# Kernel optimization log

Measured on AMD Instinct MI355X. Metric: run time of the kernel, lower is better.

## Reference

```python
import jax, jax.numpy as jnp
import numpy as np

S, V, L = 64, 16, 5            # hn_dim=(64,16), num_layers=5
ED, RD, TD = 16, 16, 64        # edge_dim, rbf_dim, t_dim
N, EL, EG, B = 16384, 131072, 262144, 64
FIN = 2 * S + RD + ED          # per-edge message input width
H = S + 2 * V                  # message output: scalar msg + 2 vector gates
CUT_L, CUT_G = 3.0, 10.0


def _ln(x, g, b, eps=1e-5):
    m = x.mean(-1, keepdims=True)
    var = ((x - m) ** 2).mean(-1, keepdims=True)
    return (x - m) / jnp.sqrt(var + eps) * g + b


def _seg_mean(x, idx, n):
    s = jax.ops.segment_sum(x, idx, num_segments=n)
    c = jax.ops.segment_sum(jnp.ones((x.shape[0], 1), x.dtype), idx, num_segments=n)
    return s / jnp.maximum(c, 1.0)


def _edge_geom(ei, pos, cutoff):
    src, tgt = ei[0], ei[1]
    r = pos[tgt] - pos[src]                       # [E,3]
    d = jnp.sqrt(jnp.clip((r * r).sum(-1), 1e-6))
    rn = r / d[:, None]
    centers = jnp.linspace(0.0, cutoff, RD)
    width = cutoff / RD
    env = jnp.where(d < cutoff, 0.5 * (jnp.cos(jnp.pi * d / cutoff) + 1.0), 0.0)
    rbf = jnp.exp(-0.5 * ((d[:, None] - centers) / width) ** 2) * env[:, None]
    return src, tgt, rn, rbf


def setup_inputs() -> dict:
    key = jax.random.key(0)
    ks = iter(jax.random.split(key, 32))
    nrm = lambda shp, sc=1.0: jax.random.normal(next(ks), shp, jnp.float32) * sc
    x = jax.random.randint(next(ks), (N, 3), 0, 16)
    t = nrm((B, TD))
    pos = nrm((N, 3))
    eil = jax.random.randint(next(ks), (2, EL), 0, N)
    eig = jax.random.randint(next(ks), (2, EG), 0, N)
    eal = jax.random.randint(next(ks), (EL,), 0, 5)
    eag = jax.random.randint(next(ks), (EG,), 0, 5)
    batch = jnp.sort(jax.random.randint(next(ks), (N,), 0, B))
    return dict(
        x=x, t=t, pos=pos,
        edge_index_local=eil, edge_index_global=eig,
        edge_attr_local=eal, edge_attr_global=eag, batch=batch,
        atom_emb=nrm((3, 16, S), 0.1),
        bond_emb=nrm((5, ED), 0.1),
        t_w1=nrm((TD, TD), TD ** -0.5), t_b1=jnp.zeros(TD),
        t_w2=nrm((TD, S), TD ** -0.5), t_b2=jnp.zeros(S),
        gnn_wm=nrm((L, 2, FIN, H), FIN ** -0.5), gnn_bm=jnp.zeros((L, 2, H)),
        gnn_wu=nrm((L, 2, S, S), S ** -0.5), gnn_bu=jnp.zeros((L, 2, S)),
        ln_g=jnp.ones((L, S)), ln_b=jnp.zeros((L, S)),
        head_dscore_w=nrm((S, 1), S ** -0.5),
        head_out_w=nrm((V, 1), V ** -0.5),
    )


def reference(x, t, pos, edge_index_local, edge_index_global, edge_attr_local,
              edge_attr_global, batch, atom_emb, bond_emb, t_w1, t_b1, t_w2,
              t_b2, gnn_wm, gnn_bm, gnn_wu, gnn_bu, ln_g, ln_b,
              head_dscore_w, head_out_w):
    n = x.shape[0]
    # AtomEncoder: sum of per-feature-column embeddings; + broadcast t-embedding
    s = atom_emb[0][x[:, 0]] + atom_emb[1][x[:, 1]] + atom_emb[2][x[:, 2]]
    temb = jax.nn.silu(jax.nn.silu(t @ t_w1 + t_b1) @ t_w2 + t_b2)
    s = s + temb[batch]
    v = jnp.zeros((n, 3, V), s.dtype)

    edge_sets = []
    for ei, ea, cut in ((edge_index_local, edge_attr_local, CUT_L),
                        (edge_index_global, edge_attr_global, CUT_G)):
        src, tgt, rn, rbf = _edge_geom(ei, pos, cut)
        edge_sets.append((src, tgt, rn, rbf, bond_emb[ea]))

    for i in range(L):
        for k, (src, tgt, rn, rbf, e) in enumerate(edge_sets):
            feat = jnp.concatenate([s[src], s[tgt], rbf, e], -1)       # [E,FIN]
            h = jax.nn.silu(feat @ gnn_wm[i, k] + gnn_bm[i, k])        # [E,H]
            ms, wv1, wv2 = h[:, :S], h[:, S:S + V], h[:, S + V:]
            vm = v[src] * wv1[:, None, :] + rn[:, :, None] * wv2[:, None, :]
            agg_s = _seg_mean(ms, tgt, n)                              # [N,S]
            agg_v = _seg_mean(vm.reshape(-1, 3 * V), tgt, n).reshape(n, 3, V)
            s = s + jax.nn.silu(agg_s @ gnn_wu[i, k] + gnn_bu[i, k])
            v = v + agg_v
        s = _ln(s, ln_g[i], ln_b[i])

    # ScoreHead (conservative=False)
    dsc = jax.nn.silu(s) @ head_dscore_w                               # [N,1]
    src, tgt = edge_index_global[0], edge_index_global[1]
    sr = (dsc[src] + dsc[tgt]) * (pos[src] - pos[tgt])                 # [E,3]
    sr = jax.ops.segment_sum(sr, tgt, num_segments=n)                  # [N,3]
    score = (v @ head_out_w)[..., 0] + sr                              # [N,3]
    return score
```

## Files before the change

kernel.cpp:

```cpp
#include <hip/hip_runtime.h>
#include <math.h>

#define Sdim 64
#define Vdim 16
#define NLAYER 5
#define EDdim 16
#define RDdim 16
#define TDdim 64
#define FINdim 160
#define Hdim 96
#define NVdim 48
#define ACCW 113
#define HPAD 98
#define VSW 52
#define GW 16

typedef __attribute__((ext_vector_type(8))) short bf16x8;
typedef __attribute__((ext_vector_type(4))) float f32x4;

__device__ __forceinline__ float silu_f(float x) {
    return x / (1.0f + __expf(-x));
}

__device__ __forceinline__ unsigned short f2bf(float x) {
    union { float f; unsigned u; } v; v.f = x;
    unsigned r = v.u + 0x7fffu + ((v.u >> 16) & 1u);
    return (unsigned short)(r >> 16);
}

__global__ __launch_bounds__(256) void pack_kernel(
    const float* __restrict__ wm, const float* __restrict__ bemb,
    unsigned short* __restrict__ wp, unsigned short* __restrict__ bondbf)
{
    int idx = blockIdx.x * 256 + threadIdx.x;
    if (idx < 10 * FINdim * Hdim) {
        int ls = idx / (FINdim * Hdim), rem = idx % (FINdim * Hdim);
        int k = rem / Hdim, c = rem % Hdim;
        wp[(size_t)ls * FINdim * Hdim + ((size_t)(k >> 3) * Hdim + c) * 8 + (k & 7)] =
            f2bf(wm[idx]);
    } else if (idx < 10 * FINdim * Hdim + 80) {
        int i = idx - 10 * FINdim * Hdim;
        bondbf[i] = f2bf(bemb[i]);
    }
}

__global__ __launch_bounds__(64) void temb_kernel(
    const float* __restrict__ t, const float* __restrict__ w1, const float* __restrict__ b1,
    const float* __restrict__ w2, const float* __restrict__ b2, float* __restrict__ temb)
{
    int b = blockIdx.x, j = threadIdx.x;
    __shared__ float row[TDdim];
    __shared__ float hid[TDdim];
    row[j] = t[b * TDdim + j];
    __syncthreads();
    float h = b1[j];
    #pragma unroll 8
    for (int i = 0; i < TDdim; ++i) h = fmaf(row[i], w1[i * TDdim + j], h);
    h = silu_f(h);
    hid[j] = h;
    __syncthreads();
    float o = b2[j];
    #pragma unroll 8
    for (int i = 0; i < TDdim; ++i) o = fmaf(hid[i], w2[i * Sdim + j], o);
    temb[b * Sdim + j] = silu_f(o);
}

__global__ __launch_bounds__(256) void node_init_kernel(
    const int* __restrict__ x, const int* __restrict__ batch,
    const float* __restrict__ aemb, const float* __restrict__ temb,
    float* __restrict__ sfeat, unsigned short* __restrict__ sbf, int n)
{
    int idx = blockIdx.x * 256 + threadIdx.x;
    if (idx >= n * Sdim) return;
    int node = idx >> 6, j = idx & 63;
    int x0 = x[node * 3 + 0], x1 = x[node * 3 + 1], x2 = x[node * 3 + 2];
    float v = aemb[(0 * 16 + x0) * Sdim + j] + aemb[(16 + x1) * Sdim + j]
            + aemb[(32 + x2) * Sdim + j] + temb[batch[node] * Sdim + j];
    sfeat[idx] = v;
    sbf[idx]   = f2bf(v);
}

__global__ __launch_bounds__(256) void count_kernel(
    const int* __restrict__ ei, int E, int* __restrict__ counts)
{
    int e = blockIdx.x * 256 + threadIdx.x;
    if (e >= E) return;
    atomicAdd(&counts[ei[E + e]], 1);
}

__global__ __launch_bounds__(256) void scan_kernel(
    const int* __restrict__ counts, int n,
    int* __restrict__ rowStart, int* __restrict__ cursor)
{
    __shared__ int partial[256];
    __shared__ int spart[257];
    int t = threadIdx.x;
    int chunk = n / 256;
    int base = t * chunk;
    int s = 0;
    for (int i = 0; i < chunk; ++i) s += counts[base + i];
    partial[t] = s;
    __syncthreads();
    if (t == 0) {
        int a = 0;
        for (int i = 0; i < 256; ++i) { spart[i] = a; a += partial[i]; }
        spart[256] = a;
    }
    __syncthreads();
    int off = spart[t];
    for (int i = 0; i < chunk; ++i) {
        rowStart[base + i] = off;
        cursor[base + i]   = off;
        off += counts[base + i];
    }
    if (t == 255) rowStart[n] = spart[256];
}

__global__ __launch_bounds__(256) void scatter_kernel(
    const int* __restrict__ ei, const int* __restrict__ ea, int E,
    int* __restrict__ cursor, int2* __restrict__ st2, int* __restrict__ eaS)
{
    int e = blockIdx.x * 256 + threadIdx.x;
    if (e >= E) return;
    int tgt = ei[E + e];
    int p = atomicAdd(&cursor[tgt], 1);
    st2[p] = make_int2(ei[e], tgt);
    eaS[p] = ea[e];
}

__global__ __launch_bounds__(256) void geom_kernel(
    const float* __restrict__ pos,
    const int2* __restrict__ st2, const int* __restrict__ eaS,
    const unsigned short* __restrict__ bondbf,
    float4* __restrict__ rn4, unsigned short* __restrict__ rbfb,
    int E, float cutoff)
{
    int e = blockIdx.x * 256 + threadIdx.x;
    if (e >= E) return;
    int2 st = st2[e];
    int s = st.x, t = st.y;
    float rx = pos[3*t]-pos[3*s], ry = pos[3*t+1]-pos[3*s+1], rz = pos[3*t+2]-pos[3*s+2];
    float d = sqrtf(fmaxf(rx*rx + ry*ry + rz*rz, 1e-6f));
    float invd = 1.0f / d;
    rn4[e] = make_float4(rx*invd, ry*invd, rz*invd, d);
    float env = (d < cutoff) ? 0.5f * (__cosf(3.14159265358979f * d / cutoff) + 1.0f) : 0.0f;
    float invw = (float)RDdim / cutoff;
    unsigned int pk[8];
    #pragma unroll
    for (int i2 = 0; i2 < 8; ++i2) {
        float c0 = cutoff * ((float)(2*i2)     / 15.0f);
        float c1 = cutoff * ((float)(2*i2 + 1) / 15.0f);
        float t0 = (d - c0) * invw, t1 = (d - c1) * invw;
        unsigned short b0 = f2bf(__expf(-0.5f * t0 * t0) * env);
        unsigned short b1 = f2bf(__expf(-0.5f * t1 * t1) * env);
        pk[i2] = (unsigned)b0 | ((unsigned)b1 << 16);
    }
    uint4* o = reinterpret_cast<uint4*>(rbfb + (size_t)e * 32);
    o[0] = make_uint4(pk[0], pk[1], pk[2], pk[3]);
    o[1] = make_uint4(pk[4], pk[5], pk[6], pk[7]);
    int ea = eaS[e];
    const uint4* bp = reinterpret_cast<const uint4*>(bondbf + ea * EDdim);
    o[2] = bp[0];
    o[3] = bp[1];
}

__global__ __launch_bounds__(192, 4) void fused_layer_tri(
    const float* __restrict__ s_in, float* __restrict__ s_out,
    const unsigned short* __restrict__ sbf_in, unsigned short* __restrict__ sbf_out,
    const float* __restrict__ v_in, float* __restrict__ v_out,
    const int* __restrict__ rowStart,
    const int2* __restrict__ st2,
    const float4* __restrict__ rn4, const unsigned short* __restrict__ rbfb,
    const unsigned short* __restrict__ wp, const float* __restrict__ bg,
    const float* __restrict__ wu, const float* __restrict__ bu,
    const float* __restrict__ lng, const float* __restrict__ lnb,
    int do_ln)
{
    __shared__ float accL[GW * ACCW];
    __shared__ __align__(16) float hS[16 * HPAD];
    __shared__ __align__(16) float vS[16 * VSW];
    __shared__ __align__(16) float rnS[16 * 4];
    __shared__ int rsW[3][GW + 1];

    const int tid  = threadIdx.x;
    const int lane = tid & 63;
    const int wid  = __builtin_amdgcn_readfirstlane(tid >> 6);
    const int l15  = lane & 15, l4 = lane >> 4;
    const int n0   = blockIdx.x * GW;

    bf16x8 B0[5], B1[5];
    #pragma unroll
    for (int kk = 0; kk < 5; ++kk) {
        B0[kk] = *reinterpret_cast<const bf16x8*>(
            wp + ((size_t)(kk * 4 + l4) * Hdim + (wid * 2 + 0) * 16 + l15) * 8);
        B1[kk] = *reinterpret_cast<const bf16x8*>(
            wp + ((size_t)(kk * 4 + l4) * Hdim + (wid * 2 + 1) * 16 + l15) * 8);
    }
    const float bias0 = bg[(wid * 2 + 0) * 16 + l15];
    const float bias1 = bg[(wid * 2 + 1) * 16 + l15];

    if (wid < 2) {
        if (lane < 32)
            #pragma unroll
            for (int i = 0; i < GW; ++i) accL[i * ACCW + wid * 32 + lane] = 0.0f;
    } else if (lane < 49) {
        #pragma unroll
        for (int i = 0; i < GW; ++i) accL[i * ACCW + 64 + lane] = 0.0f;
    }
    if (lane <= GW) rsW[wid][lane] = rowStart[n0 + lane];

    const int eW0 = __builtin_amdgcn_readfirstlane(rsW[wid][0]);
    const int eW1 = __builtin_amdgcn_readfirstlane(rsW[wid][GW]);
    const int eLast = max(eW1 - 1, 0);

    auto reduceChunk = [&](int pb) {
        const int pv = min(16, eW1 - pb);
        if (wid < 2) {
            if (lane < 32) {
                const int col = wid * 32 + lane;
                for (int i = 0; i < GW; ++i) {
                    int lo = rsW[wid][i] - pb;     if (lo < 0) lo = 0;
                    int hi = rsW[wid][i + 1] - pb; if (hi > pv) hi = pv;
                    if (lo >= hi) continue;
                    float msum = 0.0f;
                    for (int e2 = lo; e2 < hi; ++e2) msum += hS[e2 * HPAD + col];
                    accL[i * ACCW + col] += msum;
                }
            }
        } else if (lane < NVdim) {
            const int m = l15, dd = l4;
            for (int i = 0; i < GW; ++i) {
                int lo = rsW[2][i] - pb;     if (lo < 0) lo = 0;
                int hi = rsW[2][i + 1] - pb; if (hi > pv) hi = pv;
                if (lo >= hi) continue;
                float vsum = 0.0f;
                for (int e2 = lo; e2 < hi; ++e2)
                    vsum += vS[e2 * VSW + lane] * hS[e2 * HPAD + 64 + m]
                          + rnS[e2 * 4 + dd]   * hS[e2 * HPAD + 80 + m];
                accL[i * ACCW + 64 + lane] += vsum;
            }
        }
    };

    int2 stM = st2[min(eW0 + l15, eLast)];
    int  sSt = 0;
    if (wid == 2) sSt = st2[min(eW0 + (lane >> 2), eLast)].x;
    int prevBase = -1;

    for (int base = eW0; base < eW1; base += 16) {
        const unsigned short* sp = sbf_in + (size_t)stM.x * Sdim;
        const unsigned short* tp = sbf_in + (size_t)stM.y * Sdim;
        bf16x8 a0 = *reinterpret_cast<const bf16x8*>(sp + l4 * 8);
        bf16x8 a1 = *reinterpret_cast<const bf16x8*>(sp + 32 + l4 * 8);
        bf16x8 a2 = *reinterpret_cast<const bf16x8*>(tp + l4 * 8);
        bf16x8 a3 = *reinterpret_cast<const bf16x8*>(tp + 32 + l4 * 8);
        bf16x8 a4 = *reinterpret_cast<const bf16x8*>(
            rbfb + (size_t)min(base + l15, eLast) * 32 + l4 * 8);

        int2 stMn = st2[min(base + 16 + l15, eLast)];
        int  sStn = 0;
        float4 va, vb, vc, rnv;
        if (wid == 2) {
            sStn = st2[min(base + 16 + (lane >> 2), eLast)].x;
            const int q = lane & 3;
            const float* vp = v_in + (size_t)sSt * NVdim + q * 12;
            va = *reinterpret_cast<const float4*>(vp);
            vb = *reinterpret_cast<const float4*>(vp + 4);
            vc = *reinterpret_cast<const float4*>(vp + 8);
            if (lane < 16) rnv = rn4[min(base + lane, eLast)];
        }

        if (prevBase >= 0) reduceChunk(prevBase);

        f32x4 c0 = (f32x4){0.f, 0.f, 0.f, 0.f};
        f32x4 c1 = (f32x4){0.f, 0.f, 0.f, 0.f};
        c0 = __builtin_amdgcn_mfma_f32_16x16x32_bf16(a0, B0[0], c0, 0, 0, 0);
        c1 = __builtin_amdgcn_mfma_f32_16x16x32_bf16(a0, B1[0], c1, 0, 0, 0);
        c0 = __builtin_amdgcn_mfma_f32_16x16x32_bf16(a1, B0[1], c0, 0, 0, 0);
        c1 = __builtin_amdgcn_mfma_f32_16x16x32_bf16(a1, B1[1], c1, 0, 0, 0);
        c0 = __builtin_amdgcn_mfma_f32_16x16x32_bf16(a2, B0[2], c0, 0, 0, 0);
        c1 = __builtin_amdgcn_mfma_f32_16x16x32_bf16(a2, B1[2], c1, 0, 0, 0);
        c0 = __builtin_amdgcn_mfma_f32_16x16x32_bf16(a3, B0[3], c0, 0, 0, 0);
        c1 = __builtin_amdgcn_mfma_f32_16x16x32_bf16(a3, B1[3], c1, 0, 0, 0);
        c0 = __builtin_amdgcn_mfma_f32_16x16x32_bf16(a4, B0[4], c0, 0, 0, 0);
        c1 = __builtin_amdgcn_mfma_f32_16x16x32_bf16(a4, B1[4], c1, 0, 0, 0);

        #pragma unroll
        for (int r = 0; r < 4; ++r) {
            hS[(l4 * 4 + r) * HPAD + wid * 32 + l15]      = silu_f(c0[r] + bias0);
            hS[(l4 * 4 + r) * HPAD + wid * 32 + 16 + l15] = silu_f(c1[r] + bias1);
        }
        if (wid == 2) {
            const int el = lane >> 2, q = lane & 3;
            *reinterpret_cast<float4*>(&vS[el * VSW + q * 12 + 0]) = va;
            *reinterpret_cast<float4*>(&vS[el * VSW + q * 12 + 4]) = vb;
            *reinterpret_cast<float4*>(&vS[el * VSW + q * 12 + 8]) = vc;
            if (lane < 16) *reinterpret_cast<float4*>(&rnS[lane * 4]) = rnv;
        }
        prevBase = base;
        stM = stMn; sSt = sStn;
    }
    if (prevBase >= 0) reduceChunk(prevBase);
    __syncthreads();

    for (int i = wid; i < GW; i += 3) {
        const int node = n0 + i;
        const float cntn = (float)(rsW[wid][i + 1] - rsW[wid][i]);
        const float ic = 1.0f / fmaxf(cntn, 1.0f);
        const float* al = &accL[i * ACCW];
        float dot = 0.0f;
        #pragma unroll 8
        for (int ii = 0; ii < Sdim; ++ii) dot = fmaf(al[ii], wu[ii * Sdim + lane], dot);
        float sn = s_in[(size_t)node * Sdim + lane] + silu_f(fmaf(dot, ic, bu[lane]));
        if (do_ln) {
            float mm = sn;
            #pragma unroll
            for (int off = 32; off >= 1; off >>= 1) mm += __shfl_xor(mm, off);
            mm *= (1.0f / 64.0f);
            float dv = sn - mm;
            float var = dv * dv;
            #pragma unroll
            for (int off = 32; off >= 1; off >>= 1) var += __shfl_xor(var, off);
            var *= (1.0f / 64.0f);
            sn = dv * rsqrtf(var + 1e-5f) * lng[lane] + lnb[lane];
        }
        s_out[(size_t)node * Sdim + lane]   = sn;
        sbf_out[(size_t)node * Sdim + lane] = f2bf(sn);
        if (lane < NVdim)
            v_out[(size_t)node * NVdim + lane] =
                v_in[(size_t)node * NVdim + lane] + accL[i * ACCW + Sdim + lane] * ic;
    }
}

__global__ __launch_bounds__(64) void head1_kernel(
    const float* __restrict__ sfeat, const float* __restrict__ vfeat,
    const float* __restrict__ wd, const float* __restrict__ wo,
    float* __restrict__ dsc, float* __restrict__ out)
{
    int node = blockIdx.x, j = threadIdx.x;
    float val = silu_f(sfeat[(size_t)node * Sdim + j]) * wd[j];
    #pragma unroll
    for (int off = 32; off >= 1; off >>= 1) val += __shfl_xor(val, off);
    if (j == 0) dsc[node] = val;
    if (j < 3) {
        float a = 0.0f;
        #pragma unroll
        for (int m = 0; m < Vdim; ++m)
            a += vfeat[(size_t)node * NVdim + j * Vdim + m] * wo[m];
        out[(size_t)node * 3 + j] = a;
    }
}

__global__ __launch_bounds__(256) void head2_kernel(
    const float* __restrict__ dsc, const float* __restrict__ pos,
    const int* __restrict__ eig, float* __restrict__ out, int E)
{
    int e = blockIdx.x * 256 + threadIdx.x;
    if (e >= E) return;
    int src = eig[e], tgt = eig[E + e];
    float w = dsc[src] + dsc[tgt];
    atomicAdd(out + 3 * tgt + 0, w * (pos[3*src+0] - pos[3*tgt+0]));
    atomicAdd(out + 3 * tgt + 1, w * (pos[3*src+1] - pos[3*tgt+1]));
    atomicAdd(out + 3 * tgt + 2, w * (pos[3*src+2] - pos[3*tgt+2]));
}

extern "C" void kernel_launch(void* const* d_in, const int* in_sizes, int n_in,
                              void* d_out, int out_size, void* d_ws, size_t ws_size,
                              hipStream_t stream)
{
    const int*   x     = (const int*)d_in[0];
    const float* t     = (const float*)d_in[1];
    const float* pos   = (const float*)d_in[2];
    const int*   eil   = (const int*)d_in[3];
    const int*   eig   = (const int*)d_in[4];
    const int*   eal   = (const int*)d_in[5];
    const int*   eag   = (const int*)d_in[6];
    const int*   batch = (const int*)d_in[7];
    const float* aemb  = (const float*)d_in[8];
    const float* bemb  = (const float*)d_in[9];
    const float* t_w1  = (const float*)d_in[10];
    const float* t_b1  = (const float*)d_in[11];
    const float* t_w2  = (const float*)d_in[12];
    const float* t_b2  = (const float*)d_in[13];
    const float* wm    = (const float*)d_in[14];
    const float* bm    = (const float*)d_in[15];
    const float* wu    = (const float*)d_in[16];
    const float* bu    = (const float*)d_in[17];
    const float* lng   = (const float*)d_in[18];
    const float* lnb   = (const float*)d_in[19];
    const float* wd    = (const float*)d_in[20];
    const float* wo    = (const float*)d_in[21];

    const int n  = in_sizes[7];
    const int B  = in_sizes[1] / TDdim;
    const int EL = in_sizes[3] / 2;
    const int EG = in_sizes[4] / 2;

    char* p = (char*)d_ws;
    auto alignup = [](char* q) { return (char*)(((size_t)q + 15) & ~(size_t)15); };

    float* temb = (float*)p;                 p += (size_t)B * Sdim * 4;
    float* dsc  = (float*)p;                 p += (size_t)n * 4;
    float* sA   = (float*)p;                 p += (size_t)n * Sdim * 4;
    float* sB   = (float*)p;                 p += (size_t)n * Sdim * 4;
    float* vA   = (float*)p;                 p += (size_t)n * NVdim * 4;
    float* vB   = (float*)p;                 p += (size_t)n * NVdim * 4;
    int* counts = (int*)p;                   p += (size_t)n * 4;
    int* cursor = (int*)p;                   p += (size_t)n * 4;
    int* rsL    = (int*)p;                   p += (size_t)(n + 4) * 4;
    int* rsG    = (int*)p;                   p += (size_t)(n + 4) * 4;
    int* eaL2   = (int*)p;                   p += (size_t)EL * 4;
    int* eaG2   = (int*)p;                   p += (size_t)EG * 4;
    p = alignup(p);
    int2* st2L  = (int2*)p;                  p += (size_t)EL * 8;
    int2* st2G  = (int2*)p;                  p += (size_t)EG * 8;
    p = alignup(p);
    unsigned short* wp     = (unsigned short*)p;  p += (size_t)10 * FINdim * Hdim * 2;
    p = alignup(p);
    unsigned short* bondbf = (unsigned short*)p;  p += 96 * 2;
    p = alignup(p);
    unsigned short* sbfA   = (unsigned short*)p;  p += (size_t)n * Sdim * 2;
    unsigned short* sbfB   = (unsigned short*)p;  p += (size_t)n * Sdim * 2;
    p = alignup(p);
    float4* rn4L = (float4*)p;               p += (size_t)EL * 16;
    float4* rn4G = (float4*)p;               p += (size_t)EG * 16;
    unsigned short* rbfbL = (unsigned short*)p;  p += (size_t)EL * 32 * 2;
    unsigned short* rbfbG = (unsigned short*)p;  p += (size_t)EG * 32 * 2;

    float* out = (float*)d_out;

    pack_kernel<<<(10 * FINdim * Hdim + 80 + 255) / 256, 256, 0, stream>>>(wm, bemb, wp, bondbf);
    temb_kernel<<<B, 64, 0, stream>>>(t, t_w1, t_b1, t_w2, t_b2, temb);
    node_init_kernel<<<(n * Sdim + 255) / 256, 256, 0, stream>>>(x, batch, aemb, temb, sA, sbfA, n);
    hipMemsetAsync(vA, 0, (size_t)n * NVdim * sizeof(float), stream);

    hipMemsetAsync(counts, 0, (size_t)n * sizeof(int), stream);
    count_kernel<<<(EL + 255) / 256, 256, 0, stream>>>(eil, EL, counts);
    scan_kernel<<<1, 256, 0, stream>>>(counts, n, rsL, cursor);
    scatter_kernel<<<(EL + 255) / 256, 256, 0, stream>>>(eil, eal, EL, cursor, st2L, eaL2);

    hipMemsetAsync(counts, 0, (size_t)n * sizeof(int), stream);
    count_kernel<<<(EG + 255) / 256, 256, 0, stream>>>(eig, EG, counts);
    scan_kernel<<<1, 256, 0, stream>>>(counts, n, rsG, cursor);
    scatter_kernel<<<(EG + 255) / 256, 256, 0, stream>>>(eig, eag, EG, cursor, st2G, eaG2);

    geom_kernel<<<(EL + 255) / 256, 256, 0, stream>>>(pos, st2L, eaL2, bondbf, rn4L, rbfbL, EL, 3.0f);
    geom_kernel<<<(EG + 255) / 256, 256, 0, stream>>>(pos, st2G, eaG2, bondbf, rn4G, rbfbG, EG, 10.0f);

    float* s_cur = sA; float* s_nxt = sB;
    float* v_cur = vA; float* v_nxt = vB;
    unsigned short* sb_cur = sbfA; unsigned short* sb_nxt = sbfB;

    for (int l = 0; l < NLAYER; ++l) {
        for (int k = 0; k < 2; ++k) {
            int ls = l * 2 + k;
            const unsigned short* wpk = wp + (size_t)ls * FINdim * Hdim;
            const float* bgk = bm + (size_t)ls * Hdim;
            const float* wuk = wu + (size_t)ls * Sdim * Sdim;
            const float* buk = bu + (size_t)ls * Sdim;
            if (k == 0) {
                fused_layer_tri<<<n / GW, 192, 0, stream>>>(
                    s_cur, s_nxt, sb_cur, sb_nxt, v_cur, v_nxt,
                    rsL, st2L, rn4L, rbfbL, wpk, bgk, wuk, buk,
                    lng + (size_t)l * Sdim, lnb + (size_t)l * Sdim, 0);
            } else {
                fused_layer_tri<<<n / GW, 192, 0, stream>>>(
                    s_cur, s_nxt, sb_cur, sb_nxt, v_cur, v_nxt,
                    rsG, st2G, rn4G, rbfbG, wpk, bgk, wuk, buk,
                    lng + (size_t)l * Sdim, lnb + (size_t)l * Sdim, 1);
            }
            float* tmp = s_cur; s_cur = s_nxt; s_nxt = tmp;
            tmp = v_cur; v_cur = v_nxt; v_nxt = tmp;
            unsigned short* tb = sb_cur; sb_cur = sb_nxt; sb_nxt = tb;
        }
    }

    head1_kernel<<<n, 64, 0, stream>>>(s_cur, v_cur, wd, wo, dsc, out);
    head2_kernel<<<(EG + 255) / 256, 256, 0, stream>>>(dsc, pos, eig, out, EG);
}
```

Baseline: 731.5 us.

## Halve node group size, keep row offsets in registers, use CSR head gather

Shrinks the per-block node group from 16 to 8, which doubles the number of blocks for the fused layer kernel. Row offsets now live in wave-uniform registers instead of shared memory, and the reduction loops are unrolled. The scan kernel uses a wave-level shuffle prefix instead of a serial loop in one thread. The final score head now walks the sorted CSR edges per node and reuses the stored unit vectors and distances instead of issuing atomics per edge. This relies on rn4.w holding the edge distance with the correct sign, and more blocks means weight fragments are reloaded more often.

```diff
diff --git a/kernel.cpp b/kernel.cpp
--- a/kernel.cpp
+++ b/kernel.cpp
@@ -13,7 +13,7 @@
 #define ACCW 113
 #define HPAD 98
 #define VSW 52
-#define GW 16
+#define GW 8
 
 typedef __attribute__((ext_vector_type(8))) short bf16x8;
 typedef __attribute__((ext_vector_type(4))) float f32x4;
@@ -92,28 +92,30 @@
     const int* __restrict__ counts, int n,
     int* __restrict__ rowStart, int* __restrict__ cursor)
 {
-    __shared__ int partial[256];
-    __shared__ int spart[257];
+    __shared__ int wsum[4];
     int t = threadIdx.x;
     int chunk = n / 256;
     int base = t * chunk;
     int s = 0;
     for (int i = 0; i < chunk; ++i) s += counts[base + i];
-    partial[t] = s;
+    int lane = t & 63, w = t >> 6;
+    int sc = s;
+    #pragma unroll
+    for (int off = 1; off < 64; off <<= 1) {
+        int xv = __shfl_up(sc, off);
+        if (lane >= off) sc += xv;
+    }
+    if (lane == 63) wsum[w] = sc;
     __syncthreads();
-    if (t == 0) {
-        int a = 0;
-        for (int i = 0; i < 256; ++i) { spart[i] = a; a += partial[i]; }
-        spart[256] = a;
-    }
-    __syncthreads();
-    int off = spart[t];
+    int woff = 0;
+    for (int i = 0; i < w; ++i) woff += wsum[i];
+    int off = woff + sc - s;
     for (int i = 0; i < chunk; ++i) {
         rowStart[base + i] = off;
         cursor[base + i]   = off;
         off += counts[base + i];
     }
-    if (t == 255) rowStart[n] = spart[256];
+    if (t == 255) rowStart[n] = off;
 }
 
 __global__ __launch_bounds__(256) void scatter_kernel(
@@ -180,7 +182,6 @@
     __shared__ __align__(16) float hS[16 * HPAD];
     __shared__ __align__(16) float vS[16 * VSW];
     __shared__ __align__(16) float rnS[16 * 4];
-    __shared__ int rsW[3][GW + 1];
 
     const int tid  = threadIdx.x;
     const int lane = tid & 63;
@@ -196,8 +197,16 @@
         B1[kk] = *reinterpret_cast<const bf16x8*>(
             wp + ((size_t)(kk * 4 + l4) * Hdim + (wid * 2 + 1) * 16 + l15) * 8);
     }
+    #pragma unroll
+    for (int kk = 0; kk < 5; ++kk)
+        asm volatile("" : "+v"(B0[kk]), "+v"(B1[kk]));
     const float bias0 = bg[(wid * 2 + 0) * 16 + l15];
     const float bias1 = bg[(wid * 2 + 1) * 16 + l15];
+
+    int rs[GW + 1];
+    #pragma unroll
+    for (int i = 0; i <= GW; ++i)
+        rs[i] = __builtin_amdgcn_readfirstlane(rowStart[n0 + i]);
 
     if (wid < 2) {
         if (lane < 32)
@@ -207,10 +216,9 @@
         #pragma unroll
         for (int i = 0; i < GW; ++i) accL[i * ACCW + 64 + lane] = 0.0f;
     }
-    if (lane <= GW) rsW[wid][lane] = rowStart[n0 + lane];
-
-    const int eW0 = __builtin_amdgcn_readfirstlane(rsW[wid][0]);
-    const int eW1 = __builtin_amdgcn_readfirstlane(rsW[wid][GW]);
+
+    const int eW0 = rs[0];
+    const int eW1 = rs[GW];
     const int eLast = max(eW1 - 1, 0);
 
     auto reduceChunk = [&](int pb) {
@@ -218,9 +226,10 @@
         if (wid < 2) {
             if (lane < 32) {
                 const int col = wid * 32 + lane;
+                #pragma unroll
                 for (int i = 0; i < GW; ++i) {
-                    int lo = rsW[wid][i] - pb;     if (lo < 0) lo = 0;
-                    int hi = rsW[wid][i + 1] - pb; if (hi > pv) hi = pv;
+                    int lo = rs[i] - pb;     if (lo < 0) lo = 0;
+                    int hi = rs[i + 1] - pb; if (hi > pv) hi = pv;
                     if (lo >= hi) continue;
                     float msum = 0.0f;
                     for (int e2 = lo; e2 < hi; ++e2) msum += hS[e2 * HPAD + col];
@@ -229,9 +238,10 @@
             }
         } else if (lane < NVdim) {
             const int m = l15, dd = l4;
+            #pragma unroll
             for (int i = 0; i < GW; ++i) {
-                int lo = rsW[2][i] - pb;     if (lo < 0) lo = 0;
-                int hi = rsW[2][i + 1] - pb; if (hi > pv) hi = pv;
+                int lo = rs[i] - pb;     if (lo < 0) lo = 0;
+                int hi = rs[i + 1] - pb; if (hi > pv) hi = pv;
                 if (lo >= hi) continue;
                 float vsum = 0.0f;
                 for (int e2 = lo; e2 < hi; ++e2)
@@ -305,7 +315,7 @@
 
     for (int i = wid; i < GW; i += 3) {
         const int node = n0 + i;
-        const float cntn = (float)(rsW[wid][i + 1] - rsW[wid][i]);
+        const float cntn = (float)(rs[i + 1] - rs[i]);
         const float ic = 1.0f / fmaxf(cntn, 1.0f);
         const float* al = &accL[i * ACCW];
         float dot = 0.0f;
@@ -352,16 +362,24 @@
 }
 
 __global__ __launch_bounds__(256) void head2_kernel(
-    const float* __restrict__ dsc, const float* __restrict__ pos,
-    const int* __restrict__ eig, float* __restrict__ out, int E)
-{
-    int e = blockIdx.x * 256 + threadIdx.x;
-    if (e >= E) return;
-    int src = eig[e], tgt = eig[E + e];
-    float w = dsc[src] + dsc[tgt];
-    atomicAdd(out + 3 * tgt + 0, w * (pos[3*src+0] - pos[3*tgt+0]));
-    atomicAdd(out + 3 * tgt + 1, w * (pos[3*src+1] - pos[3*tgt+1]));
-    atomicAdd(out + 3 * tgt + 2, w * (pos[3*src+2] - pos[3*tgt+2]));
+    const float* __restrict__ dsc, const int* __restrict__ rsG,
+    const int2* __restrict__ st2G, const float4* __restrict__ rn4G,
+    float* __restrict__ out, int n)
+{
+    int t = blockIdx.x * 256 + threadIdx.x;
+    if (t >= n) return;
+    int lo = rsG[t], hi = rsG[t + 1];
+    float dt = dsc[t];
+    float ax = 0.f, ay = 0.f, az = 0.f;
+    for (int e = lo; e < hi; ++e) {
+        float w = dsc[st2G[e].x] + dt;
+        float4 rn = rn4G[e];
+        float wd_ = w * rn.w;
+        ax -= wd_ * rn.x; ay -= wd_ * rn.y; az -= wd_ * rn.z;
+    }
+    out[3 * t + 0] += ax;
+    out[3 * t + 1] += ay;
+    out[3 * t + 2] += az;
 }
 
 extern "C" void kernel_launch(void* const* d_in, const int* in_sizes, int n_in,
@@ -476,5 +494,5 @@
     }
 
     head1_kernel<<<n, 64, 0, stream>>>(s_cur, v_cur, wd, wo, dsc, out);
-    head2_kernel<<<(EG + 255) / 256, 256, 0, stream>>>(dsc, pos, eig, out, EG);
-}
+    head2_kernel<<<(n + 255) / 256, 256, 0, stream>>>(dsc, rsG, st2G, rn4G, out, n);
+}
```

New measurement: 662.8 us. 9.4% less time.
